# Performance work log

Hardware: AMD Instinct MI355X
Metric: run time of the kernel (lower is better)

The kernel has to match this reference:

```python
import jax, jax.numpy as jnp
import numpy as np

B, S, D = 2, 2048, 1024      # batch, seq, d_model
H, DH = 16, 64               # heads, head_dim
E, F, K = 16, 256, 2         # n_experts, expert_size, top_k


def setup_inputs() -> dict:
    key = jax.random.key(0)
    ks = jax.random.split(key, 12)
    w = lambda k, shape: (jax.random.normal(k, shape, jnp.float32) * 0.02)
    return {
        "hidden_states": jax.random.normal(ks[0], (B, S, D), jnp.float32),
        "Wq": w(ks[1], (D, D)),
        "Wk": w(ks[2], (D, D)),
        "Wv": w(ks[3], (D, D)),
        "Wo": w(ks[4], (D, D)),
        "ln1_scale": jnp.ones((D,), jnp.float32),
        "ln1_bias": jnp.zeros((D,), jnp.float32),
        "ln2_scale": jnp.ones((D,), jnp.float32),
        "ln2_bias": jnp.zeros((D,), jnp.float32),
        "W_sel": w(ks[5], (D, E)),
        "W1": w(ks[6], (E, D, F)),
        "W2": w(ks[7], (E, F, D)),
    }


def _layernorm(x, scale, bias, eps=1e-5):
    mu = jnp.mean(x, axis=-1, keepdims=True)
    var = jnp.mean(jnp.square(x - mu), axis=-1, keepdims=True)
    return (x - mu) * jax.lax.rsqrt(var + eps) * scale + bias


def reference(hidden_states, Wq, Wk, Wv, Wo, ln1_scale, ln1_bias,
              ln2_scale, ln2_bias, W_sel, W1, W2):
    x = hidden_states
    # ---- self-attention sublayer (pre-LN, residual) ----
    h = _layernorm(x, ln1_scale, ln1_bias)
    q = (h @ Wq).reshape(B, S, H, DH)
    k = (h @ Wk).reshape(B, S, H, DH)
    v = (h @ Wv).reshape(B, S, H, DH)
    scores = jnp.einsum("bqhd,bkhd->bhqk", q, k) / np.float32(np.sqrt(DH))
    attn = jax.nn.softmax(scores, axis=-1)
    ctx = jnp.einsum("bhqk,bkhd->bqhd", attn, v).reshape(B, S, D)
    x = x + ctx @ Wo

    # ---- SigmaMoE FFN sublayer (pre-LN, residual) ----
    h = _layernorm(x, ln2_scale, ln2_bias).reshape(B * S, D)  # [T, D]
    sel = jax.nn.sigmoid(h @ W_sel)                            # [T, E]
    vals, idx = jax.lax.top_k(sel, K)                          # [T, K]
    T = B * S
    gates = jnp.zeros((T, E), h.dtype).at[jnp.arange(T)[:, None], idx].set(vals)
    # expert MLPs, gate applied to each expert's output
    up = jax.nn.relu(jnp.einsum("td,edf->tef", h, W1))         # [T, E, F]
    up = up * gates[:, :, None]
    moe_out = jnp.einsum("tef,efd->td", up, W2).reshape(B, S, D)
    return x + moe_out
```

## Files before the change

kernel.cpp:

```cpp
#include <hip/hip_runtime.h>

typedef unsigned short u16;
typedef __attribute__((ext_vector_type(8))) short s16x8;
typedef __attribute__((ext_vector_type(4))) float f32x4;

typedef __attribute__((address_space(3))) unsigned int lds_u32_t;
typedef __attribute__((address_space(1))) unsigned int glb_u32_t;

__device__ __forceinline__ float bf2f(u16 u) {
    union { unsigned int i; float f; } c; c.i = ((unsigned int)u) << 16; return c.f;
}
__device__ __forceinline__ u16 f2bf(float f) {
    union { float f; unsigned int u; } c; c.f = f;
    unsigned int u = c.u;
    unsigned int r = (u + 0x7fffu + ((u >> 16) & 1u)) >> 16;
    return (u16)r;
}
__device__ __forceinline__ void glds16(const u16* g, short* l) {
    __builtin_amdgcn_global_load_lds((glb_u32_t*)g, (lds_u32_t*)l, 16, 0, 0);
}

__global__ __launch_bounds__(256) void transpose_split_kernel(const float* __restrict__ src,
                                                              u16* __restrict__ dh,
                                                              u16* __restrict__ dl,
                                                              int R, int C) {
    __shared__ float tile[32][33];
    int c0 = blockIdx.x * 32, r0 = blockIdx.y * 32;
    int tx = threadIdx.x & 31, ty = threadIdx.x >> 5;
    for (int i = 0; i < 4; i++)
        tile[ty + 8 * i][tx] = src[(size_t)(r0 + ty + 8 * i) * C + c0 + tx];
    __syncthreads();
    for (int i = 0; i < 4; i++) {
        float v = tile[tx][ty + 8 * i];
        u16 hb = f2bf(v);
        size_t idx = (size_t)(c0 + ty + 8 * i) * R + r0 + tx;
        dh[idx] = hb;
        dl[idx] = f2bf(v - bf2f(hb));
    }
}

__global__ __launch_bounds__(256) void transpose_f2b_kernel(const float* __restrict__ src,
                                                            u16* __restrict__ dst,
                                                            int R, int C) {
    __shared__ float tile[32][33];
    size_t zoff = (size_t)blockIdx.z * R * C;
    int c0 = blockIdx.x * 32, r0 = blockIdx.y * 32;
    int tx = threadIdx.x & 31, ty = threadIdx.x >> 5;
    for (int i = 0; i < 4; i++)
        tile[ty + 8 * i][tx] = src[zoff + (size_t)(r0 + ty + 8 * i) * C + c0 + tx];
    __syncthreads();
    for (int i = 0; i < 4; i++)
        dst[zoff + (size_t)(c0 + ty + 8 * i) * R + r0 + tx] = f2bf(tile[tx][ty + 8 * i]);
}

__global__ __launch_bounds__(256) void ln_split_kernel(const float* __restrict__ x,
                                                       const float* __restrict__ sc,
                                                       const float* __restrict__ bi,
                                                       u16* __restrict__ oh,
                                                       u16* __restrict__ ol) {
    int row = blockIdx.x, tid = threadIdx.x;
    f32x4 u = *(const f32x4*)(x + (size_t)row * 1024 + tid * 4);
    float s = u[0] + u[1] + u[2] + u[3];
    float ss = u[0]*u[0] + u[1]*u[1] + u[2]*u[2] + u[3]*u[3];
    for (int off = 1; off < 64; off <<= 1) { s += __shfl_xor(s, off, 64); ss += __shfl_xor(ss, off, 64); }
    __shared__ float red[8];
    if ((tid & 63) == 0) { red[tid >> 6] = s; red[4 + (tid >> 6)] = ss; }
    __syncthreads();
    s = red[0] + red[1] + red[2] + red[3];
    ss = red[4] + red[5] + red[6] + red[7];
    float mu = s * (1.0f / 1024.0f);
    float rstd = rsqrtf(ss * (1.0f / 1024.0f) - mu * mu + 1e-5f);
    f32x4 g = *(const f32x4*)(sc + tid * 4);
    f32x4 b = *(const f32x4*)(bi + tid * 4);
    size_t o = (size_t)row * 1024 + tid * 4;
    for (int i = 0; i < 4; i++) {
        float v = (u[i] - mu) * rstd * g[i] + b[i];
        u16 hb = f2bf(v);
        oh[o + i] = hb;
        ol[o + i] = f2bf(v - bf2f(hb));
    }
}

__global__ __launch_bounds__(256) void ln_f2b_kernel(const float* __restrict__ x,
                                                     const float* __restrict__ sc,
                                                     const float* __restrict__ bi,
                                                     u16* __restrict__ out) {
    int row = blockIdx.x, tid = threadIdx.x;
    f32x4 u = *(const f32x4*)(x + (size_t)row * 1024 + tid * 4);
    float s = u[0] + u[1] + u[2] + u[3];
    float ss = u[0]*u[0] + u[1]*u[1] + u[2]*u[2] + u[3]*u[3];
    for (int off = 1; off < 64; off <<= 1) { s += __shfl_xor(s, off, 64); ss += __shfl_xor(ss, off, 64); }
    __shared__ float red[8];
    if ((tid & 63) == 0) { red[tid >> 6] = s; red[4 + (tid >> 6)] = ss; }
    __syncthreads();
    s = red[0] + red[1] + red[2] + red[3];
    ss = red[4] + red[5] + red[6] + red[7];
    float mu = s * (1.0f / 1024.0f);
    float rstd = rsqrtf(ss * (1.0f / 1024.0f) - mu * mu + 1e-5f);
    f32x4 g = *(const f32x4*)(sc + tid * 4);
    f32x4 b = *(const f32x4*)(bi + tid * 4);
    u16* op = out + (size_t)row * 1024 + tid * 4;
    for (int i = 0; i < 4; i++)
        op[i] = f2bf((u[i] - mu) * rstd * g[i] + b[i]);
}

__global__ __launch_bounds__(256) void gemm3_qkv(const u16* __restrict__ Ah_g,
                                                 const u16* __restrict__ Al_g,
                                                 const u16* __restrict__ Bh_g,
                                                 const u16* __restrict__ Bl_g,
                                                 u16* __restrict__ Ch, u16* __restrict__ Cl,
                                                 float scale) {
    const int K = 1024;
    __shared__ __align__(16) short Ahs[128 * 32], Als[128 * 32];
    __shared__ __align__(16) short Bhs[128 * 32], Bls[128 * 32];
    int m0 = blockIdx.y * 128, n0 = blockIdx.x * 128;
    int tid = threadIdx.x, lane = tid & 63, w = tid >> 6;
    int wm = (w & 1) * 64, wn = (w >> 1) * 64;
    int lr = lane & 15, lq = lane >> 4;
    int r0 = w * 32 + (lane >> 2);
    int cv = (lane & 3) * 8;
    const u16* pAh = Ah_g + (size_t)(m0 + r0) * K + cv;
    const u16* pAl = Al_g + (size_t)(m0 + r0) * K + cv;
    const u16* pBh = Bh_g + (size_t)(n0 + r0) * K + cv;
    const u16* pBl = Bl_g + (size_t)(n0 + r0) * K + cv;
    size_t st16 = (size_t)16 * K;
    f32x4 acc[4][4] = {};

    for (int k0 = 0; k0 < K; k0 += 32) {
        glds16(pAh + k0, &Ahs[w * 1024]);  glds16(pAh + k0 + st16, &Ahs[w * 1024 + 512]);
        glds16(pAl + k0, &Als[w * 1024]);  glds16(pAl + k0 + st16, &Als[w * 1024 + 512]);
        glds16(pBh + k0, &Bhs[w * 1024]);  glds16(pBh + k0 + st16, &Bhs[w * 1024 + 512]);
        glds16(pBl + k0, &Bls[w * 1024]);  glds16(pBl + k0 + st16, &Bls[w * 1024 + 512]);
        __syncthreads();
        s16x8 ah[4], al[4], bh[4], bl[4];
        #pragma unroll
        for (int i = 0; i < 4; i++) {
            int off = (wm + i * 16 + lr) * 32 + lq * 8;
            ah[i] = *(const s16x8*)&Ahs[off];
            al[i] = *(const s16x8*)&Als[off];
        }
        #pragma unroll
        for (int j = 0; j < 4; j++) {
            int off = (wn + j * 16 + lr) * 32 + lq * 8;
            bh[j] = *(const s16x8*)&Bhs[off];
            bl[j] = *(const s16x8*)&Bls[off];
        }
        #pragma unroll
        for (int i = 0; i < 4; i++)
            #pragma unroll
            for (int j = 0; j < 4; j++) {
                acc[i][j] = __builtin_amdgcn_mfma_f32_16x16x32_bf16(al[i], bh[j], acc[i][j], 0, 0, 0);
                acc[i][j] = __builtin_amdgcn_mfma_f32_16x16x32_bf16(ah[i], bl[j], acc[i][j], 0, 0, 0);
                acc[i][j] = __builtin_amdgcn_mfma_f32_16x16x32_bf16(ah[i], bh[j], acc[i][j], 0, 0, 0);
            }
        __syncthreads();
    }

    int seg = n0 >> 10;
    float sc = (seg == 0) ? scale : 1.0f;
    u16* Chp = Ch + (size_t)seg * 8388608;
    u16* Clp = Cl + (size_t)seg * 8388608;
    int c0 = (n0 & 1023) + wn;
    #pragma unroll
    for (int i = 0; i < 4; i++)
        #pragma unroll
        for (int j = 0; j < 4; j++)
            #pragma unroll
            for (int r = 0; r < 4; r++) {
                int row = m0 + wm + i * 16 + lq * 4 + r;
                int col = c0 + j * 16 + lr;
                float vv = acc[i][j][r] * sc;
                u16 hb = f2bf(vv);
                u16 lb = f2bf(vv - bf2f(hb));
                size_t idx = (size_t)row * 1024 + col;
                Chp[idx] = hb; Clp[idx] = lb;
            }
}

__global__ __launch_bounds__(256) void gemm3_res(const u16* __restrict__ Ah_g,
                                                 const u16* __restrict__ Al_g,
                                                 const u16* __restrict__ Bh_g,
                                                 const u16* __restrict__ Bl_g,
                                                 float* __restrict__ C,
                                                 const float* __restrict__ res) {
    const int K = 1024, N = 1024;
    __shared__ __align__(16) short Ahs[128 * 32], Als[128 * 32];
    __shared__ __align__(16) short Bhs[128 * 32], Bls[128 * 32];
    int m0 = blockIdx.y * 128, n0 = blockIdx.x * 128;
    int tid = threadIdx.x, lane = tid & 63, w = tid >> 6;
    int wm = (w & 1) * 64, wn = (w >> 1) * 64;
    int lr = lane & 15, lq = lane >> 4;
    int r0 = w * 32 + (lane >> 2);
    int cv = (lane & 3) * 8;
    const u16* pAh = Ah_g + (size_t)(m0 + r0) * K + cv;
    const u16* pAl = Al_g + (size_t)(m0 + r0) * K + cv;
    const u16* pBh = Bh_g + (size_t)(n0 + r0) * K + cv;
    const u16* pBl = Bl_g + (size_t)(n0 + r0) * K + cv;
    size_t st16 = (size_t)16 * K;
    f32x4 acc[4][4] = {};

    for (int k0 = 0; k0 < K; k0 += 32) {
        glds16(pAh + k0, &Ahs[w * 1024]);  glds16(pAh + k0 + st16, &Ahs[w * 1024 + 512]);
        glds16(pAl + k0, &Als[w * 1024]);  glds16(pAl + k0 + st16, &Als[w * 1024 + 512]);
        glds16(pBh + k0, &Bhs[w * 1024]);  glds16(pBh + k0 + st16, &Bhs[w * 1024 + 512]);
        glds16(pBl + k0, &Bls[w * 1024]);  glds16(pBl + k0 + st16, &Bls[w * 1024 + 512]);
        __syncthreads();
        s16x8 ah[4], al[4], bh[4], bl[4];
        #pragma unroll
        for (int i = 0; i < 4; i++) {
            int off = (wm + i * 16 + lr) * 32 + lq * 8;
            ah[i] = *(const s16x8*)&Ahs[off];
            al[i] = *(const s16x8*)&Als[off];
        }
        #pragma unroll
        for (int j = 0; j < 4; j++) {
            int off = (wn + j * 16 + lr) * 32 + lq * 8;
            bh[j] = *(const s16x8*)&Bhs[off];
            bl[j] = *(const s16x8*)&Bls[off];
        }
        #pragma unroll
        for (int i = 0; i < 4; i++)
            #pragma unroll
            for (int j = 0; j < 4; j++) {
                acc[i][j] = __builtin_amdgcn_mfma_f32_16x16x32_bf16(al[i], bh[j], acc[i][j], 0, 0, 0);
                acc[i][j] = __builtin_amdgcn_mfma_f32_16x16x32_bf16(ah[i], bl[j], acc[i][j], 0, 0, 0);
                acc[i][j] = __builtin_amdgcn_mfma_f32_16x16x32_bf16(ah[i], bh[j], acc[i][j], 0, 0, 0);
            }
        __syncthreads();
    }

    #pragma unroll
    for (int i = 0; i < 4; i++)
        #pragma unroll
        for (int j = 0; j < 4; j++)
            #pragma unroll
            for (int r = 0; r < 4; r++) {
                int row = m0 + wm + i * 16 + lq * 4 + r;
                int col = n0 + wn + j * 16 + lr;
                size_t idx = (size_t)row * N + col;
                C[idx] = acc[i][j][r] + res[idx];
            }
}

__global__ __launch_bounds__(256) void init_out_kernel(const float* __restrict__ x2,
                                                       float* __restrict__ out) {
    size_t i = ((size_t)blockIdx.x * 256 + threadIdx.x) * 4;
    *(f32x4*)(out + i) = *(const f32x4*)(x2 + i);
}

__global__ __launch_bounds__(256) void gemm_moe_up_sparse(const u16* __restrict__ h2,
                                                          const u16* __restrict__ W1T,
                                                          const int* __restrict__ cnt,
                                                          const int* __restrict__ list,
                                                          const float* __restrict__ gates,
                                                          u16* __restrict__ up_buf) {
    const int K = 1024;
    __shared__ __align__(16) short As[128 * 32];
    __shared__ __align__(16) short Bs[128 * 32];
    int e = -1, tstart = 0;
    {
        int ty = blockIdx.y, at = 0;
        for (int i = 0; i < 16; i++) {
            int nt = (cnt[i] + 127) >> 7;
            if (ty < at + nt) { e = i; tstart = (ty - at) * 128; break; }
            at += nt;
        }
    }
    if (e < 0) return;
    int ncnt = cnt[e];
    int n0 = blockIdx.x * 128;
    int tid = threadIdx.x, lane = tid & 63, w = tid >> 6;
    int wm = (w & 1) * 64, wn = (w >> 1) * 64;
    int lr = lane & 15, lq = lane >> 4;
    int r0 = w * 32 + (lane >> 2);
    int cv = (lane & 3) * 8;
    int p0 = tstart + r0, p1 = tstart + r0 + 16;
    int t0 = list[e * 4096 + (p0 < ncnt ? p0 : ncnt - 1)];
    int t1 = list[e * 4096 + (p1 < ncnt ? p1 : ncnt - 1)];
    const u16* pA0 = h2 + (size_t)t0 * K + cv;
    const u16* pA1 = h2 + (size_t)t1 * K + cv;
    const u16* pB  = W1T + (size_t)(e * 256 + n0 + r0) * K + cv;
    size_t st16 = (size_t)16 * K;
    f32x4 acc[4][4] = {};

    for (int k0 = 0; k0 < K; k0 += 32) {
        glds16(pA0 + k0, &As[w * 1024]);  glds16(pA1 + k0, &As[w * 1024 + 512]);
        glds16(pB + k0, &Bs[w * 1024]);   glds16(pB + k0 + st16, &Bs[w * 1024 + 512]);
        __syncthreads();
        s16x8 av[4], bv[4];
        #pragma unroll
        for (int i = 0; i < 4; i++) av[i] = *(const s16x8*)&As[(wm + i * 16 + lr) * 32 + lq * 8];
        #pragma unroll
        for (int j = 0; j < 4; j++) bv[j] = *(const s16x8*)&Bs[(wn + j * 16 + lr) * 32 + lq * 8];
        #pragma unroll
        for (int i = 0; i < 4; i++)
            #pragma unroll
            for (int j = 0; j < 4; j++)
                acc[i][j] = __builtin_amdgcn_mfma_f32_16x16x32_bf16(av[i], bv[j], acc[i][j], 0, 0, 0);
        __syncthreads();
    }

    #pragma unroll
    for (int i = 0; i < 4; i++)
        #pragma unroll
        for (int j = 0; j < 4; j++)
            #pragma unroll
            for (int r = 0; r < 4; r++) {
                int rl = wm + i * 16 + lq * 4 + r;
                int p = tstart + rl;
                if (p < ncnt) {
                    int t = list[e * 4096 + p];
                    float g = gates[(size_t)t * 16 + e];
                    int col = n0 + wn + j * 16 + lr;
                    up_buf[(size_t)(e * 4096 + p) * 256 + col] = f2bf(fmaxf(acc[i][j][r], 0.0f) * g);
                }
            }
}

__global__ __launch_bounds__(256) void gemm_moe_down_sparse(const u16* __restrict__ up_buf,
                                                            const u16* __restrict__ W2T,
                                                            const int* __restrict__ cnt,
                                                            const int* __restrict__ list,
                                                            float* __restrict__ out) {
    const int K = 256;
    __shared__ __align__(16) short As[128 * 32];
    __shared__ __align__(16) short Bs[128 * 32];
    int e = -1, tstart = 0;
    {
        int ty = blockIdx.y, at = 0;
        for (int i = 0; i < 16; i++) {
            int nt = (cnt[i] + 127) >> 7;
            if (ty < at + nt) { e = i; tstart = (ty - at) * 128; break; }
            at += nt;
        }
    }
    if (e < 0) return;
    int ncnt = cnt[e];
    int n0 = blockIdx.x * 128;
    int tid = threadIdx.x, lane = tid & 63, w = tid >> 6;
    int wm = (w & 1) * 64, wn = (w >> 1) * 64;
    int lr = lane & 15, lq = lane >> 4;
    int r0 = w * 32 + (lane >> 2);
    int cv = (lane & 3) * 8;
    int p0 = tstart + r0, p1 = tstart + r0 + 16;
    int pc0 = p0 < ncnt ? p0 : ncnt - 1;
    int pc1 = p1 < ncnt ? p1 : ncnt - 1;
    const u16* pA0 = up_buf + (size_t)(e * 4096 + pc0) * 256 + cv;
    const u16* pA1 = up_buf + (size_t)(e * 4096 + pc1) * 256 + cv;
    const u16* pB  = W2T + (size_t)(n0 + r0) * 4096 + e * 256 + cv;
    size_t st16 = (size_t)16 * 4096;
    f32x4 acc[4][4] = {};

    for (int k0 = 0; k0 < K; k0 += 32) {
        glds16(pA0 + k0, &As[w * 1024]);  glds16(pA1 + k0, &As[w * 1024 + 512]);
        glds16(pB + k0, &Bs[w * 1024]);   glds16(pB + k0 + st16, &Bs[w * 1024 + 512]);
        __syncthreads();
        s16x8 av[4], bv[4];
        #pragma unroll
        for (int i = 0; i < 4; i++) av[i] = *(const s16x8*)&As[(wm + i * 16 + lr) * 32 + lq * 8];
        #pragma unroll
        for (int j = 0; j < 4; j++) bv[j] = *(const s16x8*)&Bs[(wn + j * 16 + lr) * 32 + lq * 8];
        #pragma unroll
        for (int i = 0; i < 4; i++)
            #pragma unroll
            for (int j = 0; j < 4; j++)
                acc[i][j] = __builtin_amdgcn_mfma_f32_16x16x32_bf16(av[i], bv[j], acc[i][j], 0, 0, 0);
        __syncthreads();
    }

    #pragma unroll
    for (int i = 0; i < 4; i++)
        #pragma unroll
        for (int j = 0; j < 4; j++)
            #pragma unroll
            for (int r = 0; r < 4; r++) {
                int rl = wm + i * 16 + lq * 4 + r;
                int p = tstart + rl;
                if (p < ncnt) {
                    int t = list[e * 4096 + p];
                    int col = n0 + wn + j * 16 + lr;
                    atomicAdd(&out[(size_t)t * 1024 + col], acc[i][j][r]);
                }
            }
}

__global__ __launch_bounds__(256) void vtrans_kernel(const u16* __restrict__ v_hi,
                                                     const u16* __restrict__ v_lo,
                                                     u16* __restrict__ vT_hi,
                                                     u16* __restrict__ vT_lo) {
    __shared__ __align__(16) short tile[64][72];
    int st = blockIdx.x, bh = blockIdx.y;
    int b = bh >> 4, h = bh & 15;
    int tid = threadIdx.x;
    int i = tid >> 2, seg = (tid & 3) * 16;
    for (int p = 0; p < 2; p++) {
        const u16* src = p ? v_lo : v_hi;
        u16* dst = p ? vT_lo : vT_hi;
        size_t goff = (size_t)(b * 2048 + st * 64 + i) * 1024 + h * 64 + seg;
        *(s16x8*)&tile[i][seg]     = *(const s16x8*)&src[goff];
        *(s16x8*)&tile[i][seg + 8] = *(const s16x8*)&src[goff + 8];
        __syncthreads();
        s16x8 o0, o1;
        for (int j = 0; j < 8; j++) { o0[j] = tile[seg + j][i]; o1[j] = tile[seg + 8 + j][i]; }
        size_t doff = ((size_t)bh * 64 + i) * 2048 + st * 64 + seg;
        *(s16x8*)&dst[doff]     = o0;
        *(s16x8*)&dst[doff + 8] = o1;
        __syncthreads();
    }
}

__global__ __launch_bounds__(256) void attn_mfma(const u16* __restrict__ qh_g,
                                                 const u16* __restrict__ ql_g,
                                                 const u16* __restrict__ kh_g,
                                                 const u16* __restrict__ kl_g,
                                                 const u16* __restrict__ vth_g,
                                                 const u16* __restrict__ vtl_g,
                                                 u16* __restrict__ ch_g,
                                                 u16* __restrict__ cl_g) {
    __shared__ __align__(16) short Ksh[64][72], Ksl[64][72], Vsh[64][72], Vsl[64][72];
    __shared__ __align__(16) short Ph[4][16 * 64], Pl[4][16 * 64];
    int lin = blockIdx.x + 16 * blockIdx.y;
    int xcd = lin & 7, rest = lin >> 3;
    int qt = rest & 15;
    int bh = xcd + 8 * (rest >> 4);
    int b = bh >> 4, h = bh & 15;
    int tid = threadIdx.x, w = tid >> 6, lane = tid & 63;
    int lr = lane & 15, lq = lane >> 4;
    int qbase = qt * 128 + w * 32;

    s16x8 qfh[2][2], qfl[2][2];
    for (int rt = 0; rt < 2; rt++)
        for (int kc = 0; kc < 2; kc++) {
            size_t qoff = (size_t)(b * 2048 + qbase + rt * 16 + lr) * 1024 + h * 64 + kc * 32 + lq * 8;
            qfh[rt][kc] = *(const s16x8*)&qh_g[qoff];
            qfl[rt][kc] = *(const s16x8*)&ql_g[qoff];
        }

    float m_[2][4], l_[2][4];
    f32x4 O[2][4] = {};
    for (int rt = 0; rt < 2; rt++)
        for (int r = 0; r < 4; r++) { m_[rt][r] = -1e30f; l_[rt][r] = 0.0f; }

    for (int kc0 = 0; kc0 < 2048; kc0 += 64) {
        {
            int kk = tid >> 2, seg = (tid & 3) * 16;
            size_t goff = (size_t)(b * 2048 + kc0 + kk) * 1024 + h * 64 + seg;
            *(s16x8*)&Ksh[kk][seg]     = *(const s16x8*)&kh_g[goff];
            *(s16x8*)&Ksh[kk][seg + 8] = *(const s16x8*)&kh_g[goff + 8];
            *(s16x8*)&Ksl[kk][seg]     = *(const s16x8*)&kl_g[goff];
            *(s16x8*)&Ksl[kk][seg + 8] = *(const s16x8*)&kl_g[goff + 8];
            size_t voff = ((size_t)bh * 64 + kk) * 2048 + kc0 + seg;
            *(s16x8*)&Vsh[kk][seg]     = *(const s16x8*)&vth_g[voff];
            *(s16x8*)&Vsh[kk][seg + 8] = *(const s16x8*)&vth_g[voff + 8];
            *(s16x8*)&Vsl[kk][seg]     = *(const s16x8*)&vtl_g[voff];
            *(s16x8*)&Vsl[kk][seg + 8] = *(const s16x8*)&vtl_g[voff + 8];
        }
        __syncthreads();

        f32x4 s[2][4] = {};
        for (int ct = 0; ct < 4; ct++)
            for (int kc = 0; kc < 2; kc++) {
                s16x8 kbh = *(const s16x8*)&Ksh[ct * 16 + lr][kc * 32 + lq * 8];
                s16x8 kbl = *(const s16x8*)&Ksl[ct * 16 + lr][kc * 32 + lq * 8];
                for (int rt = 0; rt < 2; rt++) {
                    s[rt][ct] = __builtin_amdgcn_mfma_f32_16x16x32_bf16(qfl[rt][kc], kbh, s[rt][ct], 0, 0, 0);
                    s[rt][ct] = __builtin_amdgcn_mfma_f32_16x16x32_bf16(qfh[rt][kc], kbl, s[rt][ct], 0, 0, 0);
                    s[rt][ct] = __builtin_amdgcn_mfma_f32_16x16x32_bf16(qfh[rt][kc], kbh, s[rt][ct], 0, 0, 0);
                }
            }

        for (int rt = 0; rt < 2; rt++) {
            float al[4];
            for (int ri = 0; ri < 4; ri++) {
                float mx = fmaxf(fmaxf(s[rt][0][ri], s[rt][1][ri]), fmaxf(s[rt][2][ri], s[rt][3][ri]));
                for (int off = 1; off < 16; off <<= 1) mx = fmaxf(mx, __shfl_xor(mx, off, 64));
                float mn = fmaxf(m_[rt][ri], mx);
                float a = __expf(m_[rt][ri] - mn);
                m_[rt][ri] = mn; al[ri] = a;
                float ps = 0.0f;
                for (int ct = 0; ct < 4; ct++) {
                    float p = __expf(s[rt][ct][ri] - mn);
                    s[rt][ct][ri] = p; ps += p;
                }
                for (int off = 1; off < 16; off <<= 1) ps += __shfl_xor(ps, off, 64);
                l_[rt][ri] = l_[rt][ri] * a + ps;
            }
            for (int nt = 0; nt < 4; nt++)
                for (int ri = 0; ri < 4; ri++) O[rt][nt][ri] *= al[ri];
            for (int ct = 0; ct < 4; ct++)
                for (int ri = 0; ri < 4; ri++) {
                    float p = s[rt][ct][ri];
                    u16 hb = f2bf(p);
                    u16 lb = f2bf(p - bf2f(hb));
                    int row = lq * 4 + ri, col = ct * 16 + lr;
                    int pidx = (row * 64 + col) ^ ((row & 7) << 3);
                    Ph[w][pidx] = (short)hb;
                    Pl[w][pidx] = (short)lb;
                }
            asm volatile("s_waitcnt lgkmcnt(0)" ::: "memory");
            __builtin_amdgcn_sched_barrier(0);
            __builtin_amdgcn_s_setprio(1);
            for (int kc = 0; kc < 2; kc++) {
                int pidx = (lr * 64 + kc * 32 + lq * 8) ^ ((lr & 7) << 3);
                s16x8 pah = *(const s16x8*)&Ph[w][pidx];
                s16x8 pal = *(const s16x8*)&Pl[w][pidx];
                for (int nt = 0; nt < 4; nt++) {
                    s16x8 vbh = *(const s16x8*)&Vsh[nt * 16 + lr][kc * 32 + lq * 8];
                    s16x8 vbl = *(const s16x8*)&Vsl[nt * 16 + lr][kc * 32 + lq * 8];
                    O[rt][nt] = __builtin_amdgcn_mfma_f32_16x16x32_bf16(pal, vbh, O[rt][nt], 0, 0, 0);
                    O[rt][nt] = __builtin_amdgcn_mfma_f32_16x16x32_bf16(pah, vbl, O[rt][nt], 0, 0, 0);
                    O[rt][nt] = __builtin_amdgcn_mfma_f32_16x16x32_bf16(pah, vbh, O[rt][nt], 0, 0, 0);
                }
            }
            __builtin_amdgcn_s_setprio(0);
            asm volatile("s_waitcnt lgkmcnt(0)" ::: "memory");
            __builtin_amdgcn_sched_barrier(0);
        }
        __syncthreads();
    }

    for (int rt = 0; rt < 2; rt++)
        for (int nt = 0; nt < 4; nt++)
            for (int ri = 0; ri < 4; ri++) {
                int row = qbase + rt * 16 + lq * 4 + ri;
                int d = nt * 16 + lr;
                float v = O[rt][nt][ri] / l_[rt][ri];
                u16 hb = f2bf(v);
                size_t idx = (size_t)(b * 2048 + row) * 1024 + h * 64 + d;
                ch_g[idx] = hb;
                cl_g[idx] = f2bf(v - bf2f(hb));
            }
}

__global__ __launch_bounds__(256) void router_kernel(const float* __restrict__ x2,
                                                     const float* __restrict__ sc,
                                                     const float* __restrict__ bi,
                                                     const float* __restrict__ Wsel,
                                                     float* __restrict__ gates,
                                                     int* __restrict__ cnt,
                                                     int* __restrict__ list) {
    int tid = threadIdx.x, w = tid >> 6, lane = tid & 63;
    int t = blockIdx.x * 4 + w;
    const float* xp = x2 + (size_t)t * 1024;
    float s = 0.0f, ss = 0.0f;
    for (int i = 0; i < 16; i++) {
        float v = xp[lane * 16 + i];
        s += v; ss += v * v;
    }
    for (int off = 1; off < 64; off <<= 1) { s += __shfl_xor(s, off, 64); ss += __shfl_xor(ss, off, 64); }
    float mu = s * (1.0f / 1024.0f);
    float rstd = rsqrtf(ss * (1.0f / 1024.0f) - mu * mu + 1e-5f);
    int e = lane & 15, part = lane >> 4;
    float acc = 0.0f;
    for (int d = part * 256; d < part * 256 + 256; d++) {
        float h = (xp[d] - mu) * rstd * sc[d] + bi[d];
        acc += h * Wsel[(size_t)d * 16 + e];
    }
    acc += __shfl_xor(acc, 16, 64);
    acc += __shfl_xor(acc, 32, 64);
    float v = 1.0f / (1.0f + __expf(-acc));
    float m1 = v;
    for (int off = 1; off < 64; off <<= 1) m1 = fmaxf(m1, __shfl_xor(m1, off, 64));
    unsigned long long b1 = __ballot(v == m1);
    int e1 = (__ffsll(b1) - 1) & 15;
    float v2 = (e == e1) ? -1e30f : v;
    float m2 = v2;
    for (int off = 1; off < 64; off <<= 1) m2 = fmaxf(m2, __shfl_xor(m2, off, 64));
    unsigned long long b2 = __ballot(v2 == m2);
    int e2 = (__ffsll(b2) - 1) & 15;
    if (lane < 16)
        gates[(size_t)t * 16 + e] = (e == e1) ? m1 : (e == e2 ? m2 : 0.0f);
    if (lane == 0) {
        int p1 = atomicAdd(&cnt[e1], 1);
        list[e1 * 4096 + p1] = t;
        int p2 = atomicAdd(&cnt[e2], 1);
        list[e2 * 4096 + p2] = t;
    }
}

extern "C" void kernel_launch(void* const* d_in, const int* in_sizes, int n_in,
                              void* d_out, int out_size, void* d_ws, size_t ws_size,
                              hipStream_t stream) {
    const float* x    = (const float*)d_in[0];
    const float* Wq   = (const float*)d_in[1];
    const float* Wk   = (const float*)d_in[2];
    const float* Wv   = (const float*)d_in[3];
    const float* Wo   = (const float*)d_in[4];
    const float* ln1s = (const float*)d_in[5];
    const float* ln1b = (const float*)d_in[6];
    const float* ln2s = (const float*)d_in[7];
    const float* ln2b = (const float*)d_in[8];
    const float* Wsel = (const float*)d_in[9];
    const float* W1   = (const float*)d_in[10];
    const float* W2   = (const float*)d_in[11];
    float* out = (float*)d_out;

    char* ws = (char*)d_ws;
    const size_t MB = 1024 * 1024;
    u16*   h1_h  = (u16*)  (ws + 0 * MB);
    u16*   h1_l  = (u16*)  (ws + 8 * MB);
    u16*   vT_hi = (u16*)  (ws + 0 * MB);
    u16*   vT_lo = (u16*)  (ws + 8 * MB);
    u16*   h2    = (u16*)  (ws + 0 * MB);
    float* gates = (float*)(ws + 8 * MB);
    int*   cnt   = (int*)  (ws + 9 * MB);
    int*   list  = (int*)  (ws + 9 * MB + 4096);
    u16*   q_hi  = (u16*)  (ws + 16 * MB);
    u16*   q_lo  = (u16*)  (ws + 24 * MB);
    u16*   k_hi  = (u16*)  (ws + 32 * MB);
    u16*   k_lo  = (u16*)  (ws + 40 * MB);
    u16*   up    = (u16*)  (ws + 16 * MB);
    u16*   v_hi  = (u16*)  (ws + 48 * MB);
    u16*   v_lo  = (u16*)  (ws + 56 * MB);
    u16*   ctx_h = (u16*)  (ws + 48 * MB);
    u16*   ctx_l = (u16*)  (ws + 56 * MB);
    float* x2    = (float*)(ws + 64 * MB);
    u16*   WqT_h = (u16*)  (ws + 80 * MB);
    u16*   WkT_h = (u16*)  (ws + 82 * MB);
    u16*   WvT_h = (u16*)  (ws + 84 * MB);
    u16*   WqT_l = (u16*)  (ws + 86 * MB);
    u16*   WkT_l = (u16*)  (ws + 88 * MB);
    u16*   WvT_l = (u16*)  (ws + 90 * MB);
    u16*   WoT_h = (u16*)  (ws + 92 * MB);
    u16*   WoT_l = (u16*)  (ws + 94 * MB);
    u16*   W1T   = (u16*)  (ws + 80 * MB);
    u16*   W2T   = (u16*)  (ws + 88 * MB);

    transpose_split_kernel<<<dim3(32, 32), 256, 0, stream>>>(Wq, WqT_h, WqT_l, 1024, 1024);
    transpose_split_kernel<<<dim3(32, 32), 256, 0, stream>>>(Wk, WkT_h, WkT_l, 1024, 1024);
    transpose_split_kernel<<<dim3(32, 32), 256, 0, stream>>>(Wv, WvT_h, WvT_l, 1024, 1024);
    transpose_split_kernel<<<dim3(32, 32), 256, 0, stream>>>(Wo, WoT_h, WoT_l, 1024, 1024);

    ln_split_kernel<<<4096, 256, 0, stream>>>(x, ln1s, ln1b, h1_h, h1_l);
    gemm3_qkv<<<dim3(24, 32), 256, 0, stream>>>(h1_h, h1_l, WqT_h, WqT_l, q_hi, q_lo, 0.125f);
    vtrans_kernel<<<dim3(32, 32), 256, 0, stream>>>(v_hi, v_lo, vT_hi, vT_lo);
    attn_mfma<<<dim3(16, 32), 256, 0, stream>>>(q_hi, q_lo, k_hi, k_lo, vT_hi, vT_lo, ctx_h, ctx_l);
    gemm3_res<<<dim3(8, 32), 256, 0, stream>>>(ctx_h, ctx_l, WoT_h, WoT_l, x2, x);
    ln_f2b_kernel<<<4096, 256, 0, stream>>>(x2, ln2s, ln2b, h2);
    hipMemsetAsync(cnt, 0, 16 * sizeof(int), stream);
    router_kernel<<<1024, 256, 0, stream>>>(x2, ln2s, ln2b, Wsel, gates, cnt, list);
    init_out_kernel<<<4096, 256, 0, stream>>>(x2, out);
    transpose_f2b_kernel<<<dim3(8, 32, 16), 256, 0, stream>>>(W1, W1T, 1024, 256);
    transpose_f2b_kernel<<<dim3(32, 128, 1), 256, 0, stream>>>(W2, W2T, 4096, 1024);
    gemm_moe_up_sparse<<<dim3(2, 80), 256, 0, stream>>>(h2, W1T, cnt, list, gates, up);
    gemm_moe_down_sparse<<<dim3(8, 80), 256, 0, stream>>>(up, W2T, cnt, list, out);
}
```

Measured before the change: 683.2 us.

## Replace MoE down-projection atomics with compact buffer and gather-combine kernel

The down-projection GEMM now writes per-assignment rows into a compact buffer instead of doing float atomicAdds into the output. A new gather kernel adds the residual and the two expert contributions for each token, which also replaces the separate output-initialisation kernel. The up buffer is packed by prefix-summed expert offsets rather than fixed 4096-row slots. The router records each token's (expert, position) pair so the gather can find its rows. This removes atomic contention and makes the output accumulation deterministic. The cost is an extra fp32 intermediate (8192x1024) written and read back, plus one more kernel launch.

```diff
diff --git a/kernel.cpp b/kernel.cpp
--- a/kernel.cpp
+++ b/kernel.cpp
@@ -242,12 +242,6 @@
             }
 }
 
-__global__ __launch_bounds__(256) void init_out_kernel(const float* __restrict__ x2,
-                                                       float* __restrict__ out) {
-    size_t i = ((size_t)blockIdx.x * 256 + threadIdx.x) * 4;
-    *(f32x4*)(out + i) = *(const f32x4*)(x2 + i);
-}
-
 __global__ __launch_bounds__(256) void gemm_moe_up_sparse(const u16* __restrict__ h2,
                                                           const u16* __restrict__ W1T,
                                                           const int* __restrict__ cnt,
@@ -257,13 +251,14 @@
     const int K = 1024;
     __shared__ __align__(16) short As[128 * 32];
     __shared__ __align__(16) short Bs[128 * 32];
-    int e = -1, tstart = 0;
+    int e = -1, tstart = 0, base_e = 0;
     {
-        int ty = blockIdx.y, at = 0;
+        int ty = blockIdx.y, at = 0, bs = 0;
         for (int i = 0; i < 16; i++) {
-            int nt = (cnt[i] + 127) >> 7;
-            if (ty < at + nt) { e = i; tstart = (ty - at) * 128; break; }
-            at += nt;
+            int c = cnt[i];
+            int nt = (c + 127) >> 7;
+            if (e < 0 && ty < at + nt) { e = i; tstart = (ty - at) * 128; base_e = bs; }
+            at += nt; bs += c;
         }
     }
     if (e < 0) return;
@@ -312,7 +307,7 @@
                     int t = list[e * 4096 + p];
                     float g = gates[(size_t)t * 16 + e];
                     int col = n0 + wn + j * 16 + lr;
-                    up_buf[(size_t)(e * 4096 + p) * 256 + col] = f2bf(fmaxf(acc[i][j][r], 0.0f) * g);
+                    up_buf[(size_t)(base_e + p) * 256 + col] = f2bf(fmaxf(acc[i][j][r], 0.0f) * g);
                 }
             }
 }
@@ -320,18 +315,18 @@
 __global__ __launch_bounds__(256) void gemm_moe_down_sparse(const u16* __restrict__ up_buf,
                                                             const u16* __restrict__ W2T,
                                                             const int* __restrict__ cnt,
-                                                            const int* __restrict__ list,
-                                                            float* __restrict__ out) {
+                                                            float* __restrict__ down_buf) {
     const int K = 256;
     __shared__ __align__(16) short As[128 * 32];
     __shared__ __align__(16) short Bs[128 * 32];
-    int e = -1, tstart = 0;
+    int e = -1, tstart = 0, base_e = 0;
     {
-        int ty = blockIdx.y, at = 0;
+        int ty = blockIdx.y, at = 0, bs = 0;
         for (int i = 0; i < 16; i++) {
-            int nt = (cnt[i] + 127) >> 7;
-            if (ty < at + nt) { e = i; tstart = (ty - at) * 128; break; }
-            at += nt;
+            int c = cnt[i];
+            int nt = (c + 127) >> 7;
+            if (e < 0 && ty < at + nt) { e = i; tstart = (ty - at) * 128; base_e = bs; }
+            at += nt; bs += c;
         }
     }
     if (e < 0) return;
@@ -345,8 +340,8 @@
     int p0 = tstart + r0, p1 = tstart + r0 + 16;
     int pc0 = p0 < ncnt ? p0 : ncnt - 1;
     int pc1 = p1 < ncnt ? p1 : ncnt - 1;
-    const u16* pA0 = up_buf + (size_t)(e * 4096 + pc0) * 256 + cv;
-    const u16* pA1 = up_buf + (size_t)(e * 4096 + pc1) * 256 + cv;
+    const u16* pA0 = up_buf + (size_t)(base_e + pc0) * 256 + cv;
+    const u16* pA1 = up_buf + (size_t)(base_e + pc1) * 256 + cv;
     const u16* pB  = W2T + (size_t)(n0 + r0) * 4096 + e * 256 + cv;
     size_t st16 = (size_t)16 * 4096;
     f32x4 acc[4][4] = {};
@@ -377,11 +372,33 @@
                 int rl = wm + i * 16 + lq * 4 + r;
                 int p = tstart + rl;
                 if (p < ncnt) {
-                    int t = list[e * 4096 + p];
                     int col = n0 + wn + j * 16 + lr;
-                    atomicAdd(&out[(size_t)t * 1024 + col], acc[i][j][r]);
+                    down_buf[(size_t)(base_e + p) * 1024 + col] = acc[i][j][r];
                 }
             }
+}
+
+__global__ __launch_bounds__(256) void gather_out_kernel(const float* __restrict__ x2,
+                                                         const float* __restrict__ down_buf,
+                                                         const int* __restrict__ cnt,
+                                                         const int* __restrict__ pidx,
+                                                         float* __restrict__ out) {
+    int t = blockIdx.x, tid = threadIdx.x;
+    int i1 = pidx[t * 2], i2 = pidx[t * 2 + 1];
+    int e1 = i1 >> 12, p1 = i1 & 4095;
+    int e2 = i2 >> 12, p2 = i2 & 4095;
+    int b1 = 0, b2 = 0;
+    for (int i = 0; i < 16; i++) {
+        int c = cnt[i];
+        if (i < e1) b1 += c;
+        if (i < e2) b2 += c;
+    }
+    size_t o = (size_t)t * 1024 + tid * 4;
+    f32x4 a  = *(const f32x4*)(x2 + o);
+    f32x4 c1 = *(const f32x4*)(down_buf + (size_t)(b1 + p1) * 1024 + tid * 4);
+    f32x4 c2 = *(const f32x4*)(down_buf + (size_t)(b2 + p2) * 1024 + tid * 4);
+    for (int k = 0; k < 4; k++) a[k] = a[k] + c1[k] + c2[k];
+    *(f32x4*)(out + o) = a;
 }
 
 __global__ __launch_bounds__(256) void vtrans_kernel(const u16* __restrict__ v_hi,
@@ -538,7 +555,8 @@
                                                      const float* __restrict__ Wsel,
                                                      float* __restrict__ gates,
                                                      int* __restrict__ cnt,
-                                                     int* __restrict__ list) {
+                                                     int* __restrict__ list,
+                                                     int* __restrict__ pidx) {
     int tid = threadIdx.x, w = tid >> 6, lane = tid & 63;
     int t = blockIdx.x * 4 + w;
     const float* xp = x2 + (size_t)t * 1024;
@@ -573,8 +591,10 @@
     if (lane == 0) {
         int p1 = atomicAdd(&cnt[e1], 1);
         list[e1 * 4096 + p1] = t;
+        pidx[t * 2] = (e1 << 12) | p1;
         int p2 = atomicAdd(&cnt[e2], 1);
         list[e2 * 4096 + p2] = t;
+        pidx[t * 2 + 1] = (e2 << 12) | p2;
     }
 }
 
@@ -605,11 +625,13 @@
     float* gates = (float*)(ws + 8 * MB);
     int*   cnt   = (int*)  (ws + 9 * MB);
     int*   list  = (int*)  (ws + 9 * MB + 4096);
+    int*   pidx  = (int*)  (ws + 9 * MB + 512 * 1024);
     u16*   q_hi  = (u16*)  (ws + 16 * MB);
     u16*   q_lo  = (u16*)  (ws + 24 * MB);
     u16*   k_hi  = (u16*)  (ws + 32 * MB);
     u16*   k_lo  = (u16*)  (ws + 40 * MB);
     u16*   up    = (u16*)  (ws + 16 * MB);
+    float* dbuf  = (float*)(ws + 20 * MB);
     u16*   v_hi  = (u16*)  (ws + 48 * MB);
     u16*   v_lo  = (u16*)  (ws + 56 * MB);
     u16*   ctx_h = (u16*)  (ws + 48 * MB);
@@ -638,10 +660,10 @@
     gemm3_res<<<dim3(8, 32), 256, 0, stream>>>(ctx_h, ctx_l, WoT_h, WoT_l, x2, x);
     ln_f2b_kernel<<<4096, 256, 0, stream>>>(x2, ln2s, ln2b, h2);
     hipMemsetAsync(cnt, 0, 16 * sizeof(int), stream);
-    router_kernel<<<1024, 256, 0, stream>>>(x2, ln2s, ln2b, Wsel, gates, cnt, list);
-    init_out_kernel<<<4096, 256, 0, stream>>>(x2, out);
+    router_kernel<<<1024, 256, 0, stream>>>(x2, ln2s, ln2b, Wsel, gates, cnt, list, pidx);
     transpose_f2b_kernel<<<dim3(8, 32, 16), 256, 0, stream>>>(W1, W1T, 1024, 256);
     transpose_f2b_kernel<<<dim3(32, 128, 1), 256, 0, stream>>>(W2, W2T, 4096, 1024);
     gemm_moe_up_sparse<<<dim3(2, 80), 256, 0, stream>>>(h2, W1T, cnt, list, gates, up);
-    gemm_moe_down_sparse<<<dim3(8, 80), 256, 0, stream>>>(up, W2T, cnt, list, out);
-}
+    gemm_moe_down_sparse<<<dim3(8, 80), 256, 0, stream>>>(up, W2T, cnt, dbuf);
+    gather_out_kernel<<<4096, 256, 0, stream>>>(x2, dbuf, cnt, pidx, out);
+}
```

Result: faster. 666.6 us (-2.4%).
